# Performance work log

Hardware: AMD Instinct MI355X
Metric: run time of the kernel (lower is better)

The kernel has to match this reference:

```python
import jax, jax.numpy as jnp
import numpy as np

D_MODEL = 512
STATE = 128
HALF = STATE // 2
SEQ = 4096
BATCH = 8


def setup_inputs() -> dict:
    key = jax.random.key(0)
    ks = jax.random.split(key, 4)
    u = jax.random.normal(ks[0], (BATCH, SEQ, D_MODEL), dtype=jnp.float32)
    # HiPPO init: Lambda = -0.5 + i*pi*n, n=1..HALF
    n = jnp.arange(1, HALF + 1, dtype=jnp.float32)
    log_Lambda_real = jnp.log(jnp.full((HALF,), 0.5, dtype=jnp.float32))  # log(-real) with real=-0.5
    Lambda_imag = jnp.pi * n
    B_real = jnp.ones((HALF, D_MODEL), dtype=jnp.float32)
    B_imag = jnp.zeros((HALF, D_MODEL), dtype=jnp.float32)
    C_real = jax.random.normal(ks[1], (D_MODEL, HALF), dtype=jnp.float32) / np.sqrt(STATE)
    C_imag = jax.random.normal(ks[2], (D_MODEL, HALF), dtype=jnp.float32) / np.sqrt(STATE)
    D = jax.random.normal(ks[3], (D_MODEL, D_MODEL), dtype=jnp.float32) / np.sqrt(D_MODEL)
    log_Delta = jnp.array([-3.0], dtype=jnp.float32)
    return {
        "u": u,
        "log_Lambda_real": log_Lambda_real,
        "Lambda_imag": Lambda_imag,
        "B_real": B_real,
        "B_imag": B_imag,
        "C_real": C_real,
        "C_imag": C_imag,
        "D": D,
        "log_Delta": log_Delta,
    }


def reference(u, log_Lambda_real, Lambda_imag, B_real, B_imag, C_real, C_imag, D, log_Delta):
    T = u.shape[1]
    Bc = B_real + 1j * B_imag            # (N/2, P) complex
    Cc = C_real + 1j * C_imag            # (P, N/2) complex
    # --- bilinear (Tustin) discretization ---
    Delta = jnp.exp(log_Delta)           # (1,)
    Lambda = -jnp.exp(jnp.clip(log_Lambda_real, -10.0, 10.0)) + 1j * Lambda_imag  # (N/2,)
    denom = 1.0 - (Delta / 2.0) * Lambda
    A_bar = (1.0 + (Delta / 2.0) * Lambda) / denom          # (N/2,)
    B_bar = (Delta / denom)[:, None] * Bc                   # (N/2, P)
    # --- FFT convolution with the SSM kernel k[n,t] = A_bar[n]^t ---
    t_idx = jnp.arange(T)
    k = jnp.exp(jnp.log(A_bar)[:, None] * t_idx[None, :])   # (N/2, T)
    u_c = u.astype(jnp.complex64)
    v = jnp.einsum('np,btp->bnt', B_bar, u_c)               # (B, N/2, T)
    fft_size = 2 * T
    V_f = jnp.fft.fft(v, n=fft_size, axis=-1)
    K_f = jnp.fft.fft(k, n=fft_size, axis=-1)
    conv = jnp.fft.ifft(V_f * K_f[None, :, :], axis=-1)[..., :T]  # (B, N/2, T)
    y = 2.0 * jnp.einsum('pn,bnt->btp', Cc, conv).real      # (B, T, P)
    return y + u @ D.T
```

## Files before the change

### kernel.cpp

```cpp
#include <hip/hip_runtime.h>
#include <hip/hip_bf16.h>
#include <stdint.h>


#define BATCH 8
#define SEQ   4096
#define DMODEL 512
#define HALF  64
#define CHUNK 64
#define NCHUNK (SEQ / CHUNK)
#define NT    10

typedef __attribute__((ext_vector_type(8))) short short8;
typedef __attribute__((ext_vector_type(4))) float f32x4;

__device__ __forceinline__ unsigned short f2bf(float f) {
    unsigned int u = __float_as_uint(f);
    u += 0x7fffu + ((u >> 16) & 1u);
    return (unsigned short)(u >> 16);
}
__device__ __forceinline__ float bf2f(unsigned short s) {
    return __uint_as_float((unsigned)s << 16);
}

__device__ __forceinline__ void poleA(const float* logLr, const float* Li_in,
                                      const float* logDelta, int n,
                                      float& Ar, float& Ai) {
    float Delta = expf(logDelta[0]);
    float llr = fminf(fmaxf(logLr[n], -10.f), 10.f);
    float Lr = -expf(llr);
    float Li = Li_in[n];
    float dr = 1.f - 0.5f * Delta * Lr;
    float di = -0.5f * Delta * Li;
    float dn = dr * dr + di * di;
    float nr = 1.f + 0.5f * Delta * Lr;
    float ni = 0.5f * Delta * Li;
    Ar = (nr * dr + ni * di) / dn;
    Ai = (ni * dr - nr * di) / dn;
}

#define GLOAD_LDS16(g, l)                                                    \
    __builtin_amdgcn_global_load_lds(                                        \
        (const __attribute__((address_space(1))) unsigned int*)(g),          \
        (__attribute__((address_space(3))) unsigned int*)(l), 16, 0, 0)

__global__ void k_build(const float* __restrict__ logLr, const float* __restrict__ Li_in,
                        const float* __restrict__ logDelta,
                        const float* __restrict__ Br, const float* __restrict__ Bi,
                        const float* __restrict__ Cr, const float* __restrict__ Ci,
                        const float* __restrict__ D,
                        unsigned short* __restrict__ Mv, unsigned short* __restrict__ W) {
    int bid = blockIdx.x;
    if (bid < 128) {
        int np = bid, p = threadIdx.x;
        if (p < DMODEL) {
            int n = np & 63;
            float Delta = expf(logDelta[0]);
            float llr = fminf(fmaxf(logLr[n], -10.f), 10.f);
            float Lr = -expf(llr);
            float Li = Li_in[n];
            float dr = 1.f - 0.5f * Delta * Lr;
            float di = -0.5f * Delta * Li;
            float dn = dr * dr + di * di;
            float sr = Delta * dr / dn;
            float si = -Delta * di / dn;
            float br = Br[n * DMODEL + p], bi = Bi[n * DMODEL + p];
            float v = (np < HALF) ? (sr * br - si * bi) : (si * br + sr * bi);
            Mv[np * DMODEL + p] = f2bf(v);
        }
    } else {
        int p = bid - 128, j = threadIdx.x;
        float v;
        if (j < HALF) v = 2.f * Cr[p * HALF + j];
        else if (j < 2 * HALF) v = -2.f * Ci[p * HALF + (j - HALF)];
        else v = D[p * DMODEL + (j - 2 * HALF)];
        W[p * 640 + j] = f2bf(v);
    }
}

__global__ void k_scanA(const unsigned short* __restrict__ Vb,
                        const float* __restrict__ logLr, const float* __restrict__ Li_in,
                        const float* __restrict__ logDelta,
                        float* __restrict__ E) {
    int tid = threadIdx.x;
    int n = tid & 63;
    int c = ((blockIdx.x & 31) << 1) + (tid >> 6);
    int b = blockIdx.x >> 5;
    float Ar, Ai;
    poleA(logLr, Li_in, logDelta, n, Ar, Ai);
    float xr = 0.f, xi = 0.f;
    size_t base = ((size_t)b * SEQ + (size_t)c * CHUNK) * 128 + n;
    for (int tl = 0; tl < CHUNK; ++tl) {
        float vr = bf2f(Vb[base]), vi = bf2f(Vb[base + 64]);
        float nxr = Ar * xr - Ai * xi + vr;
        float nxi = Ar * xi + Ai * xr + vi;
        xr = nxr; xi = nxi;
        base += 128;
    }
    int eidx = ((b * NCHUNK + c) * 2) * HALF + n;
    E[eidx] = xr; E[eidx + 64] = xi;
}

__global__ void k_scanCB(const unsigned short* __restrict__ Vb,
                         const float* __restrict__ E,
                         const float* __restrict__ logLr, const float* __restrict__ Li_in,
                         const float* __restrict__ logDelta,
                         unsigned short* __restrict__ Xb) {
    int tid = threadIdx.x;
    int n = tid & 63;
    int c = ((blockIdx.x & 31) << 1) + (tid >> 6);
    int b = blockIdx.x >> 5;
    float Ar, Ai;
    poleA(logLr, Li_in, logDelta, n, Ar, Ai);
    float a64r = Ar, a64i = Ai;
#pragma unroll
    for (int s = 0; s < 6; ++s) {
        float t = a64r * a64r - a64i * a64i;
        a64i = 2.f * a64r * a64i;
        a64r = t;
    }
    float xr = 0.f, xi = 0.f, wr = 1.f, wi = 0.f;
    for (int jj = 1; jj <= c; ++jj) {
        int ei = ((b * NCHUNK + (c - jj)) * 2) * HALF + n;
        float er = E[ei], ev = E[ei + 64];
        xr += wr * er - wi * ev;
        xi += wr * ev + wi * er;
        float nwr = wr * a64r - wi * a64i;
        float nwi = wr * a64i + wi * a64r;
        wr = nwr; wi = nwi;
    }
    size_t base = ((size_t)b * SEQ + (size_t)c * CHUNK) * 128 + n;
    for (int tl = 0; tl < CHUNK; ++tl) {
        float vr = bf2f(Vb[base]), vi = bf2f(Vb[base + 64]);
        float nxr = Ar * xr - Ai * xi + vr;
        float nxi = Ar * xi + Ai * xr + vi;
        xr = nxr; xi = nxi;
        Xb[base] = f2bf(xr); Xb[base + 64] = f2bf(xi);
        base += 128;
    }
}

__global__ __launch_bounds__(512) void gemm1(const float* __restrict__ U,
                                             const unsigned short* __restrict__ Mv,
                                             unsigned short* __restrict__ Vb,
                                             unsigned short* __restrict__ Ub) {
    __shared__ __align__(16) unsigned short As[64 * 32];
    __shared__ __align__(16) unsigned short Bs[128 * 32];
    const int tid = threadIdx.x;
    const int lane = tid & 63;
    const int w = tid >> 6;
    const int wm = w >> 2, wn = w & 3;
    const int l15 = lane & 15, l4 = lane >> 4;
    const int row0 = blockIdx.x * 64;
    const int srow = tid >> 3;
    const int sh = (tid & 7) * 4;

    f32x4 acc[2][2];
#pragma unroll
    for (int m = 0; m < 2; ++m)
#pragma unroll
        for (int n = 0; n < 2; ++n) acc[m][n] = (f32x4)(0.f);

    for (int k0 = 0; k0 < DMODEL; k0 += 32) {
        const float4 av = *(const float4*)(U + (size_t)(row0 + srow) * DMODEL + k0 + sh);

        __syncthreads();

        GLOAD_LDS16(Mv + (size_t)(tid >> 2) * DMODEL + k0 + (tid & 3) * 8,
                    &Bs[(w * 64) * 8]);

        uint2 wa;
        wa.x = (unsigned)f2bf(av.x) | ((unsigned)f2bf(av.y) << 16);
        wa.y = (unsigned)f2bf(av.z) | ((unsigned)f2bf(av.w) << 16);
        *(uint2*)&As[srow * 32 + sh] = wa;
        *(uint2*)&Ub[(size_t)(row0 + srow) * DMODEL + k0 + sh] = wa;

        __syncthreads();

        short8 af[2], bf[2];
#pragma unroll
        for (int m = 0; m < 2; ++m)
            af[m] = *(const short8*)&As[(wm * 32 + m * 16 + l15) * 32 + l4 * 8];
#pragma unroll
        for (int n = 0; n < 2; ++n)
            bf[n] = *(const short8*)&Bs[(wn * 32 + n * 16 + l15) * 32 + l4 * 8];
#pragma unroll
        for (int m = 0; m < 2; ++m)
#pragma unroll
            for (int n = 0; n < 2; ++n)
                acc[m][n] = __builtin_amdgcn_mfma_f32_16x16x32_bf16(af[m], bf[n], acc[m][n], 0, 0, 0);
    }

#pragma unroll
    for (int m = 0; m < 2; ++m) {
        int rbase = row0 + wm * 32 + m * 16 + l4 * 4;
#pragma unroll
        for (int n = 0; n < 2; ++n) {
            int col = wn * 32 + n * 16 + l15;
#pragma unroll
            for (int r = 0; r < 4; ++r)
                Vb[(size_t)(rbase + r) * 128 + col] = f2bf(acc[m][n][r]);
        }
    }
}


#define STAGE_K(t, kh, j) do {                                                 \
    int c_ = (kh) * 1024 + (j) * 512 + tid;                                    \
    int ct_ = c_ ^ (((c_ >> 5) & 1) << 1);                                     \
    int r_ = (ct_ >> 2) & 255;                                                 \
    int kcol_ = (t) * 64 + (kh) * 32 + (ct_ & 3) * 8;                          \
    const unsigned short* asrc_ = (kcol_ < 128)                                \
        ? Xb + (size_t)(row0 + r_) * 128 + kcol_                               \
        : Ub + (size_t)(row0 + r_) * 512 + (kcol_ - 128);                      \
    GLOAD_LDS16(asrc_, &As[((t) & 1) * 16384 + ((kh) * 1024 + (j) * 512 + w * 64) * 8]); \
    GLOAD_LDS16(W + (size_t)(col0 + r_) * 640 + kcol_,                         \
                &Bs[((t) & 1) * 16384 + ((kh) * 1024 + (j) * 512 + w * 64) * 8]); \
} while (0)

#define LDAB(t, kh) do {                                                       \
    _Pragma("unroll") for (int i_ = 0; i_ < 8; ++i_) {                         \
        int r_ = wm * 128 + i_ * 16 + l15;                                     \
        int c_ = (l4 * 8) ^ (((r_ >> 3) & 1) << 4);                            \
        af[i_] = *(const short8*)&As[((t) & 1) * 16384 + (kh) * 8192 + r_ * 32 + c_]; \
    }                                                                          \
    _Pragma("unroll") for (int j_ = 0; j_ < 4; ++j_) {                         \
        int r_ = wn * 64 + j_ * 16 + l15;                                      \
        int c_ = (l4 * 8) ^ (((r_ >> 3) & 1) << 4);                            \
        bf[j_] = *(const short8*)&Bs[((t) & 1) * 16384 + (kh) * 8192 + r_ * 32 + c_]; \
    } } while (0)

#define MFMA32() do {                                                          \
    __builtin_amdgcn_s_setprio(1);                                             \
    _Pragma("unroll") for (int i_ = 0; i_ < 8; ++i_)                           \
    _Pragma("unroll") for (int j_ = 0; j_ < 4; ++j_)                           \
        acc[i_][j_] = __builtin_amdgcn_mfma_f32_16x16x32_bf16(                 \
            af[i_], bf[j_], acc[i_][j_], 0, 0, 0);                             \
    __builtin_amdgcn_s_setprio(0);                                             \
} while (0)

#define PHASE_SYNC(N) do {                                                     \
    asm volatile("s_waitcnt vmcnt(" #N ")" ::: "memory");                      \
    __builtin_amdgcn_s_barrier();                                              \
    __builtin_amdgcn_sched_barrier(0);                                         \
} while (0)

__global__ __launch_bounds__(512) void gemm23_8p(const unsigned short* __restrict__ Xb,
                                                 const unsigned short* __restrict__ Ub,
                                                 const unsigned short* __restrict__ W,
                                                 float* __restrict__ C) {
    __shared__ __align__(16) unsigned short As[2 * 16384];
    __shared__ __align__(16) unsigned short Bs[2 * 16384];
    const int tid = threadIdx.x;
    const int lane = tid & 63;
    const int w = tid >> 6;
    const int wm = w >> 2, wn = w & 3;
    const int l15 = lane & 15, l4 = lane >> 4;

    int lin = blockIdx.y * gridDim.x + blockIdx.x;
    int sw = (lin & 7) * 32 + (lin >> 3);
    const int row0 = (sw & 127) * 256;
    const int col0 = (sw >> 7) * 256;

    f32x4 acc[8][4];
#pragma unroll
    for (int m = 0; m < 8; ++m)
#pragma unroll
        for (int n = 0; n < 4; ++n) acc[m][n] = (f32x4)(0.f);

    STAGE_K(0, 0, 0); STAGE_K(0, 0, 1);
    STAGE_K(0, 1, 0); STAGE_K(0, 1, 1);
    STAGE_K(1, 0, 0); STAGE_K(1, 0, 1);

    short8 af[8], bf[4];
    for (int t = 0; t < NT - 1; ++t) {
        PHASE_SYNC(8);
        LDAB(t, 0);
        STAGE_K(t + 1, 1, 0); STAGE_K(t + 1, 1, 1);
        MFMA32();
        PHASE_SYNC(8);
        LDAB(t, 1);
        if (t < NT - 2) { STAGE_K(t + 2, 0, 0); STAGE_K(t + 2, 0, 1); }
        MFMA32();
    }
    PHASE_SYNC(4);
    LDAB(NT - 1, 0);
    MFMA32();
    PHASE_SYNC(0);
    LDAB(NT - 1, 1);
    MFMA32();

#pragma unroll
    for (int m = 0; m < 8; ++m) {
        int rbase = row0 + wm * 128 + m * 16 + l4 * 4;
#pragma unroll
        for (int n = 0; n < 4; ++n) {
            int col = col0 + wn * 64 + n * 16 + l15;
#pragma unroll
            for (int r = 0; r < 4; ++r)
                C[(size_t)(rbase + r) * DMODEL + col] = acc[m][n][r];
        }
    }
}


extern "C" void kernel_launch(void* const* d_in, const int* in_sizes, int n_in,
                              void* d_out, int out_size, void* d_ws, size_t ws_size,
                              hipStream_t stream) {
    const float* u      = (const float*)d_in[0];
    const float* logLr  = (const float*)d_in[1];
    const float* Li     = (const float*)d_in[2];
    const float* Br     = (const float*)d_in[3];
    const float* Bi     = (const float*)d_in[4];
    const float* Cr     = (const float*)d_in[5];
    const float* Ci     = (const float*)d_in[6];
    const float* D      = (const float*)d_in[7];
    const float* logDel = (const float*)d_in[8];
    float* out = (float*)d_out;

    const size_t M = (size_t)BATCH * SEQ;
    unsigned short* Vb = (unsigned short*)d_ws;
    unsigned short* Ub = Vb + M * 128;
    unsigned short* Xb = Ub + M * 512;
    unsigned short* Mv = Xb + M * 128;
    unsigned short* W  = Mv + 128 * 512;
    float* E     = (float*)(W + 512 * 640);

    hipLaunchKernelGGL(k_build, dim3(640), dim3(640), 0, stream,
                       logLr, Li, logDel, Br, Bi, Cr, Ci, D, Mv, W);

    hipLaunchKernelGGL(gemm1, dim3(M / 64), dim3(512), 0, stream, u, Mv, Vb, Ub);

    hipLaunchKernelGGL(k_scanA, dim3(256), dim3(128), 0, stream,
                       Vb, logLr, Li, logDel, E);
    hipLaunchKernelGGL(k_scanCB, dim3(256), dim3(128), 0, stream,
                       Vb, E, logLr, Li, logDel, Xb);

    hipLaunchKernelGGL(gemm23_8p, dim3(M / 256, DMODEL / 256), dim3(512), 0, stream,
                       Xb, Ub, W, out);
}
```

Before: 79.39 us.

## Shrink final GEMM tile to 128x256 with a triple-buffered K32 pipeline

The final GEMM (X|U times W) moves from 256x256 tiles with a double-buffered K64 schedule to 128x256 tiles with a three-stage LDS ring over K32 phases, launching twice as many blocks. The aim is more blocks for the CUs, less LDS and fewer accumulator registers per block, which may allow more occupancy, plus a deeper prefetch that keeps one barrier per phase. In exchange, arithmetic intensity per block drops and W tiles are loaded twice as often.

After: 80.10 us. No clear change (+0.9%).

```diff
diff --git a/kernel.cpp b/kernel.cpp
--- a/kernel.cpp
+++ b/kernel.cpp
@@ -9,7 +9,7 @@
 #define HALF  64
 #define CHUNK 64
 #define NCHUNK (SEQ / CHUNK)
-#define NT    10
+#define NPH   20
 
 typedef __attribute__((ext_vector_type(8))) short short8;
 typedef __attribute__((ext_vector_type(4))) float f32x4;
@@ -205,34 +205,37 @@
 }
 
 
-#define STAGE_K(t, kh, j) do {                                                 \
-    int c_ = (kh) * 1024 + (j) * 512 + tid;                                    \
-    int ct_ = c_ ^ (((c_ >> 5) & 1) << 1);                                     \
-    int r_ = (ct_ >> 2) & 255;                                                 \
-    int kcol_ = (t) * 64 + (kh) * 32 + (ct_ & 3) * 8;                          \
-    const unsigned short* asrc_ = (kcol_ < 128)                                \
-        ? Xb + (size_t)(row0 + r_) * 128 + kcol_                               \
-        : Ub + (size_t)(row0 + r_) * 512 + (kcol_ - 128);                      \
-    GLOAD_LDS16(asrc_, &As[((t) & 1) * 16384 + ((kh) * 1024 + (j) * 512 + w * 64) * 8]); \
-    GLOAD_LDS16(W + (size_t)(col0 + r_) * 640 + kcol_,                         \
-                &Bs[((t) & 1) * 16384 + ((kh) * 1024 + (j) * 512 + w * 64) * 8]); \
-} while (0)
-
-#define LDAB(t, kh) do {                                                       \
-    _Pragma("unroll") for (int i_ = 0; i_ < 8; ++i_) {                         \
-        int r_ = wm * 128 + i_ * 16 + l15;                                     \
+#define STAGE_P(p) do {                                                        \
+    const int kb_ = ((p) >> 1) * 64 + ((p) & 1) * 32;                          \
+    const int s_ = (p) % 3;                                                    \
+    { int c_ = tid; int ct_ = c_ ^ (((c_ >> 5) & 1) << 1);                     \
+      int r_ = (ct_ >> 2) & 127; int kc_ = kb_ + (ct_ & 3) * 8;                \
+      const unsigned short* src_ = (kc_ < 128)                                 \
+          ? Xb + (size_t)(row0 + r_) * 128 + kc_                               \
+          : Ub + (size_t)(row0 + r_) * 512 + (kc_ - 128);                      \
+      GLOAD_LDS16(src_, &As[s_ * 4096 + (w * 64) * 8]); }                      \
+    _Pragma("unroll") for (int j_ = 0; j_ < 2; ++j_) {                         \
+      int c_ = j_ * 512 + tid; int ct_ = c_ ^ (((c_ >> 5) & 1) << 1);          \
+      int r_ = (ct_ >> 2) & 255; int kc_ = kb_ + (ct_ & 3) * 8;                \
+      GLOAD_LDS16(W + (size_t)(col0 + r_) * 640 + kc_,                         \
+                  &Bs[s_ * 8192 + (j_ * 512 + w * 64) * 8]);                   \
+    } } while (0)
+
+#define LDAB_P(p) do {                                                         \
+    const int s_ = (p) % 3;                                                    \
+    _Pragma("unroll") for (int i_ = 0; i_ < 4; ++i_) {                         \
+        int r_ = wm * 64 + i_ * 16 + l15;                                      \
         int c_ = (l4 * 8) ^ (((r_ >> 3) & 1) << 4);                            \
-        af[i_] = *(const short8*)&As[((t) & 1) * 16384 + (kh) * 8192 + r_ * 32 + c_]; \
-    }                                                                          \
+        af[i_] = *(const short8*)&As[s_ * 4096 + r_ * 32 + c_]; }              \
     _Pragma("unroll") for (int j_ = 0; j_ < 4; ++j_) {                         \
         int r_ = wn * 64 + j_ * 16 + l15;                                      \
         int c_ = (l4 * 8) ^ (((r_ >> 3) & 1) << 4);                            \
-        bf[j_] = *(const short8*)&Bs[((t) & 1) * 16384 + (kh) * 8192 + r_ * 32 + c_]; \
-    } } while (0)
-
-#define MFMA32() do {                                                          \
+        bf[j_] = *(const short8*)&Bs[s_ * 8192 + r_ * 32 + c_]; }              \
+    } while (0)
+
+#define MFMA16() do {                                                          \
     __builtin_amdgcn_s_setprio(1);                                             \
-    _Pragma("unroll") for (int i_ = 0; i_ < 8; ++i_)                           \
+    _Pragma("unroll") for (int i_ = 0; i_ < 4; ++i_)                           \
     _Pragma("unroll") for (int j_ = 0; j_ < 4; ++j_)                           \
         acc[i_][j_] = __builtin_amdgcn_mfma_f32_16x16x32_bf16(                 \
             af[i_], bf[j_], acc[i_][j_], 0, 0, 0);                             \
@@ -245,12 +248,12 @@
     __builtin_amdgcn_sched_barrier(0);                                         \
 } while (0)
 
-__global__ __launch_bounds__(512) void gemm23_8p(const unsigned short* __restrict__ Xb,
+__global__ __launch_bounds__(512) void gemm23_3s(const unsigned short* __restrict__ Xb,
                                                  const unsigned short* __restrict__ Ub,
                                                  const unsigned short* __restrict__ W,
                                                  float* __restrict__ C) {
-    __shared__ __align__(16) unsigned short As[2 * 16384];
-    __shared__ __align__(16) unsigned short Bs[2 * 16384];
+    __shared__ __align__(16) unsigned short As[3 * 4096];
+    __shared__ __align__(16) unsigned short Bs[3 * 8192];
     const int tid = threadIdx.x;
     const int lane = tid & 63;
     const int w = tid >> 6;
@@ -258,41 +261,36 @@
     const int l15 = lane & 15, l4 = lane >> 4;
 
     int lin = blockIdx.y * gridDim.x + blockIdx.x;
-    int sw = (lin & 7) * 32 + (lin >> 3);
-    const int row0 = (sw & 127) * 256;
-    const int col0 = (sw >> 7) * 256;
-
-    f32x4 acc[8][4];
-#pragma unroll
-    for (int m = 0; m < 8; ++m)
+    int sw = (lin & 7) * 64 + (lin >> 3);
+    const int row0 = (sw & 255) * 128;
+    const int col0 = (sw >> 8) * 256;
+
+    f32x4 acc[4][4];
+#pragma unroll
+    for (int m = 0; m < 4; ++m)
 #pragma unroll
         for (int n = 0; n < 4; ++n) acc[m][n] = (f32x4)(0.f);
 
-    STAGE_K(0, 0, 0); STAGE_K(0, 0, 1);
-    STAGE_K(0, 1, 0); STAGE_K(0, 1, 1);
-    STAGE_K(1, 0, 0); STAGE_K(1, 0, 1);
-
-    short8 af[8], bf[4];
-    for (int t = 0; t < NT - 1; ++t) {
-        PHASE_SYNC(8);
-        LDAB(t, 0);
-        STAGE_K(t + 1, 1, 0); STAGE_K(t + 1, 1, 1);
-        MFMA32();
-        PHASE_SYNC(8);
-        LDAB(t, 1);
-        if (t < NT - 2) { STAGE_K(t + 2, 0, 0); STAGE_K(t + 2, 0, 1); }
-        MFMA32();
-    }
-    PHASE_SYNC(4);
-    LDAB(NT - 1, 0);
-    MFMA32();
+    STAGE_P(0);
+    STAGE_P(1);
+
+    short8 af[4], bf[4];
+    for (int p = 0; p < NPH - 2; ++p) {
+        PHASE_SYNC(3);
+        LDAB_P(p);
+        STAGE_P(p + 2);
+        MFMA16();
+    }
+    PHASE_SYNC(3);
+    LDAB_P(NPH - 2);
+    MFMA16();
     PHASE_SYNC(0);
-    LDAB(NT - 1, 1);
-    MFMA32();
-
-#pragma unroll
-    for (int m = 0; m < 8; ++m) {
-        int rbase = row0 + wm * 128 + m * 16 + l4 * 4;
+    LDAB_P(NPH - 1);
+    MFMA16();
+
+#pragma unroll
+    for (int m = 0; m < 4; ++m) {
+        int rbase = row0 + wm * 64 + m * 16 + l4 * 4;
 #pragma unroll
         for (int n = 0; n < 4; ++n) {
             int col = col0 + wn * 64 + n * 16 + l15;
@@ -336,6 +334,6 @@
     hipLaunchKernelGGL(k_scanCB, dim3(256), dim3(128), 0, stream,
                        Vb, E, logLr, Li, logDel, Xb);
 
-    hipLaunchKernelGGL(gemm23_8p, dim3(M / 256, DMODEL / 256), dim3(512), 0, stream,
+    hipLaunchKernelGGL(gemm23_3s, dim3(M / 128, DMODEL / 256), dim3(512), 0, stream,
                        Xb, Ub, W, out);
 }
```
